# Kernel optimization log

Measured on AMD Instinct MI355X. Metric: run time of the kernel, lower is better.

The kernel has to match this reference:

```python
import jax, jax.numpy as jnp
import numpy as np
from jax import lax

K_NEI = 64      # max_num_neighbors in radius query
NEG = -1e30     # mask value for max-aggregation


def fps(pos, n_sample):
    """Farthest point sampling per cloud. pos: [B,N,3] -> idx [B,n_sample] int32.
    Deterministic start at point 0 (PyG uses a random start)."""
    B, N, _ = pos.shape
    start = jnp.zeros((B,), jnp.int32)
    big = jnp.full((B, N), jnp.finfo(pos.dtype).max, pos.dtype)
    def body(carry, _):
        mind, last = carry
        lp = jnp.take_along_axis(pos, last[:, None, None], axis=1)  # [B,1,3]
        d = jnp.sum((pos - lp) ** 2, -1)                            # [B,N]
        mind = jnp.minimum(mind, d)
        nxt = jnp.argmax(mind, axis=1).astype(jnp.int32)
        return (mind, nxt), nxt
    (_, _), rest = lax.scan(body, (big, start), None, length=n_sample - 1)
    return jnp.concatenate([start[None], rest], 0).T  # [B, n_sample]


def radius_nn(pos_all, pos_q, r, k):
    """Up to k nearest neighbors within radius r (per cloud).
    pos_all: [B,N,3], pos_q: [B,M,3] -> idx [B,M,k] int32, valid [B,M,k] bool."""
    d2 = jnp.sum((pos_q[:, :, None, :] - pos_all[:, None, :, :]) ** 2, -1)  # [B,M,N]
    score = jnp.where(d2 <= r * r, -d2, -jnp.inf)
    vals, idx = lax.top_k(score, k)
    return idx, jnp.isfinite(vals)


def gather(feat, idx):
    """feat: [B,P,C], idx: [B,M,k] -> [B,M,k,C]"""
    B, M, k = idx.shape
    out = jnp.take_along_axis(feat, idx.reshape(B, M * k)[:, :, None], axis=1)
    return out.reshape(B, M, k, feat.shape[-1])


def mlp3(x, w1, b1, w2, b2, w3, b3):
    x = jax.nn.relu(x @ w1 + b1)
    x = jax.nn.relu(x @ w2 + b2)
    return x @ w3 + b3


def point_conv(x, pos_src, pos_dst, nidx, valid, params):
    """PyG PointConv: message = local_nn([x_j, pos_j - pos_i]), max aggregation."""
    rel = gather(pos_src, nidx) - pos_dst[:, :, None, :]          # [B,M,k,3]
    msg = rel if x is None else jnp.concatenate([gather(x, nidx), rel], -1)
    h = mlp3(msg, *params)                                        # [B,M,k,C]
    h = jnp.where(valid[..., None], h, NEG)
    out = jnp.max(h, axis=2)
    return jnp.where(valid.any(2)[..., None], out, 0.0)


def setup_inputs() -> dict:
    key = jax.random.key(0)
    shapes = {
        'sa1_w1': (3, 64), 'sa1_b1': (64,), 'sa1_w2': (64, 64), 'sa1_b2': (64,),
        'sa1_w3': (64, 128), 'sa1_b3': (128,),
        'sa2_w1': (131, 128), 'sa2_b1': (128,), 'sa2_w2': (128, 128), 'sa2_b2': (128,),
        'sa2_w3': (128, 256), 'sa2_b3': (256,),
        'g_w1': (259, 256), 'g_b1': (256,), 'g_w2': (256, 512), 'g_b2': (512,),
        'g_w3': (512, 1024), 'g_b3': (1024,),
        'l1_w': (1024, 512), 'l1_b': (512,), 'l2_w': (512, 256), 'l2_b': (256,),
        'l3_w': (256, 7), 'l3_b': (7,),
    }
    ks = jax.random.split(key, len(shapes) + 1)
    inp = {'points': jax.random.uniform(ks[0], (8, 4096, 3), jnp.float32)}
    for i, (name, shp) in enumerate(shapes.items()):
        inp[name] = jax.random.normal(ks[i + 1], shp, jnp.float32) / np.sqrt(shp[0]).astype(np.float32)
    return inp


def reference(points, sa1_w1, sa1_b1, sa1_w2, sa1_b2, sa1_w3, sa1_b3,
              sa2_w1, sa2_b1, sa2_w2, sa2_b2, sa2_w3, sa2_b3,
              g_w1, g_b1, g_w2, g_b2, g_w3, g_b3,
              l1_w, l1_b, l2_w, l2_b, l3_w, l3_b):
    B, N, _ = points.shape
    pos = points[..., :3]
    # ---- stage 1: fps ratio 0.5, radius 0.1 ----
    N1 = N // 2
    idx1 = fps(pos, N1)
    pos1 = jnp.take_along_axis(pos, idx1[..., None], axis=1)      # [B,N1,3]
    nidx1, valid1 = radius_nn(pos, pos1, 0.1, K_NEI)
    x1 = jax.nn.relu(point_conv(None, pos, pos1, nidx1, valid1,
                                (sa1_w1, sa1_b1, sa1_w2, sa1_b2, sa1_w3, sa1_b3)))
    # ---- stage 2: fps ratio 0.25, radius 0.2 ----
    N2 = N1 // 4
    idx2 = fps(pos1, N2)
    pos2 = jnp.take_along_axis(pos1, idx2[..., None], axis=1)     # [B,N2,3]
    nidx2, valid2 = radius_nn(pos1, pos2, 0.2, K_NEI)
    x2 = jax.nn.relu(point_conv(x1, pos1, pos2, nidx2, valid2,
                                (sa2_w1, sa2_b1, sa2_w2, sa2_b2, sa2_w3, sa2_b3)))
    # ---- global MLP + grouped maxpool over 128 points ----
    g = mlp3(jnp.concatenate([x2, pos2], -1), g_w1, g_b1, g_w2, g_b2, g_w3, g_b3)  # [B,N2,1024]
    g = g.reshape(-1, 128, 1024).max(axis=1)                      # [B*N2/128, 1024]
    h = jax.nn.relu(g @ l1_w + l1_b)                              # dropout = identity (eval)
    h = jax.nn.relu(h @ l2_w + l2_b)
    h = h @ l3_w + l3_b                                           # [B*N2/128, 7]
    b_out = h.reshape(B, -1, 7).mean(axis=1)                      # [B,7]
    t = b_out[:, :3]
    q = b_out[:, 3:]
    q = q / jnp.maximum(jnp.linalg.norm(q, axis=-1, keepdims=True), 1e-12)
    return jnp.concatenate([t, q], axis=-1)
```

## Files before the change

kernel.cpp:

```cpp
#include <hip/hip_runtime.h>
#include <float.h>


typedef float f32x2 __attribute__((ext_vector_type(2)));

__device__ __forceinline__ float d2_rn(float ax, float ay, float az,
                                       float bx, float by, float bz) {
  float dx = __fsub_rn(ax, bx), dy = __fsub_rn(ay, by), dz = __fsub_rn(az, bz);
  return __fadd_rn(__fadd_rn(__fmul_rn(dx, dx), __fmul_rn(dy, dy)), __fmul_rn(dz, dz));
}

template<int CTRL>
__device__ __forceinline__ unsigned long long dppmax(unsigned long long a) {
  const unsigned int lo = (unsigned int)a, hi = (unsigned int)(a >> 32);
  const unsigned int slo =
      (unsigned int)__builtin_amdgcn_update_dpp(0, (int)lo, CTRL, 0xf, 0xf, true);
  const unsigned int shi =
      (unsigned int)__builtin_amdgcn_update_dpp(0, (int)hi, CTRL, 0xf, 0xf, true);
  const unsigned long long s = ((unsigned long long)shi << 32) | slo;
  return s > a ? s : a;
}

__device__ __forceinline__ unsigned int aload(const unsigned int* p) {
  return __hip_atomic_load(p, __ATOMIC_RELAXED, __HIP_MEMORY_SCOPE_AGENT);
}
__device__ __forceinline__ void astore(unsigned int* p, unsigned int v) {
  __hip_atomic_store(p, v, __ATOMIC_RELAXED, __HIP_MEMORY_SCOPE_AGENT);
}

__device__ __forceinline__ void barrier_lgkm() {
  asm volatile("s_waitcnt lgkmcnt(0)\n\ts_barrier" ::: "memory");
}

template<int N, int NS, int T>
__device__ void fps_core(float4* sxyz, int* s_idx,
                         unsigned long long* s_red,
                         float* __restrict__ outp,
                         unsigned int* __restrict__ pub) {
#pragma clang fp contract(off)
  constexpr int P = N / T;
  constexpr int P2 = P / 2;
  constexpr int W = T / 64;
  const int t = threadIdx.x;
  __builtin_amdgcn_s_setprio(2);
  f32x2 px[P2], py[P2], pz[P2], mind[P2];
  unsigned int kc0[P2], kc1[P2];
#pragma unroll
  for (int j = 0; j < P2; ++j) {
    const int i0 = (2*j)*T + t, i1 = i0 + T;
    const float4 c0 = sxyz[i0], c1 = sxyz[i1];
    px[j] = f32x2{c0.x, c1.x};
    py[j] = f32x2{c0.y, c1.y};
    pz[j] = f32x2{c0.z, c1.z};
    mind[j] = f32x2{FLT_MAX, FLT_MAX};
    kc0[j] = (unsigned int)(N - 1 - i0);
    kc1[j] = (unsigned int)(N - 1 - i1);
  }
  float lx = sxyz[0].x, ly = sxyz[0].y, lz = sxyz[0].z;
  if (t == 0) { s_idx[0] = 0; astore(&pub[0], 1u); }
  for (int it = 1; it < NS; ++it) {
    const f32x2 lx2 = {lx, lx}, ly2 = {ly, ly}, lz2 = {lz, lz};
    float bv0 = -1.0f, bv1 = -1.0f;
    unsigned int bk0 = 0, bk1 = 0;
#pragma unroll
    for (int j = 0; j < P2; ++j) {
      const f32x2 dx = px[j] - lx2;
      const f32x2 dy = py[j] - ly2;
      const f32x2 dz = pz[j] - lz2;
      const f32x2 s = ((dx*dx) + (dy*dy)) + (dz*dz);
      const float m0 = fminf(mind[j].x, s.x);
      const float m1 = fminf(mind[j].y, s.y);
      mind[j] = f32x2{m0, m1};
      const bool g0 = m0 > bv0;
      bv0 = g0 ? m0 : bv0; bk0 = g0 ? kc0[j] : bk0;
      const bool g1 = m1 > bv1;
      bv1 = g1 ? m1 : bv1; bk1 = g1 ? kc1[j] : bk1;
    }
    const unsigned long long k0 = ((unsigned long long)__float_as_uint(bv0) << 32) | bk0;
    const unsigned long long k1 = ((unsigned long long)__float_as_uint(bv1) << 32) | bk1;
    unsigned long long key = k0 > k1 ? k0 : k1;
    key = dppmax<0x111>(key);
    key = dppmax<0x112>(key);
    key = dppmax<0x114>(key);
    key = dppmax<0x118>(key);
    key = dppmax<0x142>(key);
    key = dppmax<0x143>(key);
    const int par = it & 1;
    if ((t & 63) == 63) s_red[par*W + (t >> 6)] = key;
    barrier_lgkm();
    unsigned long long best = s_red[par*W];
#pragma unroll
    for (int w = 1; w < W; ++w) {
      const unsigned long long o = s_red[par*W + w];
      best = o > best ? o : best;
    }
    const int idx = (N - 1) - (int)(unsigned int)(best & 0xFFFFFFFFull);
    if (t == 0) { astore(&pub[it], (unsigned int)(idx + 1)); s_idx[it] = idx; }
    const float4 c = sxyz[idx];
    lx = c.x; ly = c.y; lz = c.z;
  }
  __builtin_amdgcn_s_setprio(0);
  __syncthreads();
  for (int s = t; s < NS; s += T) {
    const float4 c = sxyz[s_idx[s]];
    outp[(size_t)s*3 + 0] = c.x; outp[(size_t)s*3 + 1] = c.y; outp[(size_t)s*3 + 2] = c.z;
  }
}

struct FpsSm { float4 xyz[4096]; int idx[2048]; unsigned long long red[8]; };
struct SmRC1 {
  union { struct { float d2[1024]; int id[1024]; } rad; float x[64 * 64]; } u;
  float rel[64 * 4];
  float out[128];
  int nid[64];
  int qidx;
  int cnt;
};
struct SmRC2 {
  union { struct { float d2[1024]; int id[1024]; } rad; float x[64 * 128]; } u;
  float rel[64 * 4];
  float out[256];
  int nid[64];
  int qidx;
  int cnt;
};
union Mega1Sm { FpsSm f; SmRC1 r; };

__device__ void rc1_item(int b, int m,
                         const float* __restrict__ points,
                         const unsigned int* __restrict__ sidx1, float r2,
                         const float* __restrict__ w1, const float* __restrict__ b1,
                         const float* __restrict__ w2, const float* __restrict__ b2,
                         const float* __restrict__ w3, const float* __restrict__ b3,
                         float* __restrict__ x1, SmRC1& R) {
  const int t = threadIdx.x;
  const int q = b*2048 + m;
  if (t == 0) {
    unsigned int v;
    while ((v = aload(&sidx1[q])) == 0u) __builtin_amdgcn_s_sleep(16);
    R.qidx = (int)v - 1;
    R.cnt = 0;
  }
  __syncthreads();
  const float* pb = points + (size_t)b * 4096 * 3;
  const int qi = R.qidx;
  const float qx = pb[qi*3], qy = pb[qi*3+1], qz = pb[qi*3+2];
  for (int i = t; i < 4096; i += 256) {
    const float d2 = d2_rn(qx, qy, qz, pb[i*3], pb[i*3+1], pb[i*3+2]);
    if (d2 <= r2) {
      const int p = atomicAdd(&R.cnt, 1);
      if (p < 1024) { R.u.rad.d2[p] = d2; R.u.rad.id[p] = i; }
    }
  }
  __syncthreads();
  const int cntc = min(R.cnt, 1024);
  const int cnt = min(cntc, 64);
  float* outp = x1 + (size_t)q * 128;
  if (cnt == 0) { if (t < 128) outp[t] = 0.f; return; }
  if (cntc <= 64) {
    if (t < cntc) R.nid[t] = R.u.rad.id[t];
  } else {
    for (int c = t; c < cntc; c += 256) {
      const float dc = R.u.rad.d2[c]; const int ic = R.u.rad.id[c];
      int rank = 0;
      for (int jj = 0; jj < cntc; ++jj)
        rank += (R.u.rad.d2[jj] < dc) || (R.u.rad.d2[jj] == dc && R.u.rad.id[jj] < ic);
      if (rank < 64) R.nid[rank] = ic;
    }
  }
  __syncthreads();
  if (t < 64) {
    const int n = (t < cnt) ? R.nid[t] : 0;
    const float* p = points + ((size_t)(b << 12) + n) * 3;
    R.rel[t*4+0] = p[0] - qx; R.rel[t*4+1] = p[1] - qy; R.rel[t*4+2] = p[2] - qz;
  }
  __syncthreads();
  const int j = t & 63;
  const int g = __builtin_amdgcn_readfirstlane(t >> 6);
  float* s_x = R.u.x;
  const int sw  = j & 31;
  const int row = j * 64;
  const float rx = R.rel[j*4+0], ry = R.rel[j*4+1], rz = R.rel[j*4+2];
  f32x2 acc[8];
  { const f32x2* bv = (const f32x2*)(b1 + g*16);
#pragma unroll
    for (int c = 0; c < 8; ++c) acc[c] = bv[c]; }
#pragma unroll
  for (int kk = 0; kk < 3; ++kk) {
    const float xk = (kk == 0) ? rx : ((kk == 1) ? ry : rz);
    const f32x2 xv = {xk, xk};
    const float4* wr = (const float4*)(w1 + kk*64 + g*16);
#pragma unroll
    for (int c4 = 0; c4 < 4; ++c4) {
      const float4 w = wr[c4];
      acc[c4*2+0] += xv * f32x2{w.x, w.y};
      acc[c4*2+1] += xv * f32x2{w.z, w.w};
    }
  }
#pragma unroll
  for (int c = 0; c < 8; ++c) {
    const f32x2 v = acc[c];
    s_x[row + ((g*16 + 2*c + 0) ^ sw)] = fmaxf(v.x, 0.f);
    s_x[row + ((g*16 + 2*c + 1) ^ sw)] = fmaxf(v.y, 0.f);
  }
  __syncthreads();
  { const f32x2* bv = (const f32x2*)(b2 + g*16);
#pragma unroll
    for (int c = 0; c < 8; ++c) acc[c] = bv[c]; }
#pragma unroll 2
  for (int k = 0; k < 64; ++k) {
    const float hk = s_x[row + (k ^ sw)];
    const f32x2 hv = {hk, hk};
    const float4* wr = (const float4*)(w2 + k*64 + g*16);
#pragma unroll
    for (int c4 = 0; c4 < 4; ++c4) {
      const float4 w = wr[c4];
      acc[c4*2+0] += hv * f32x2{w.x, w.y};
      acc[c4*2+1] += hv * f32x2{w.z, w.w};
    }
  }
  __syncthreads();
#pragma unroll
  for (int c = 0; c < 8; ++c) {
    const f32x2 v = acc[c];
    s_x[row + ((g*16 + 2*c + 0) ^ sw)] = fmaxf(v.x, 0.f);
    s_x[row + ((g*16 + 2*c + 1) ^ sw)] = fmaxf(v.y, 0.f);
  }
  __syncthreads();
#pragma unroll 1
  for (int p = 0; p < 2; ++p) {
    f32x2 a[8];
    { const f32x2* bv = (const f32x2*)(b3 + g*32 + p*16);
#pragma unroll
      for (int c = 0; c < 8; ++c) a[c] = bv[c]; }
#pragma unroll 2
    for (int k = 0; k < 64; ++k) {
      const float hk = s_x[row + (k ^ sw)];
      const f32x2 hv = {hk, hk};
      const float4* wr = (const float4*)(w3 + k*128 + g*32 + p*16);
#pragma unroll
      for (int c4 = 0; c4 < 4; ++c4) {
        const float4 w = wr[c4];
        a[c4*2+0] += hv * f32x2{w.x, w.y};
        a[c4*2+1] += hv * f32x2{w.z, w.w};
      }
    }
    if (j >= cnt) {
#pragma unroll
      for (int c = 0; c < 8; ++c) a[c] = f32x2{-1e30f, -1e30f};
    }
#pragma unroll
    for (int off = 32; off > 0; off >>= 1) {
#pragma unroll
      for (int c = 0; c < 8; ++c) {
        a[c].x = fmaxf(a[c].x, __shfl_xor(a[c].x, off, 64));
        a[c].y = fmaxf(a[c].y, __shfl_xor(a[c].y, off, 64));
      }
    }
    if (j == 0) {
#pragma unroll
      for (int c = 0; c < 8; ++c) *(f32x2*)(&R.out[g*32 + p*16 + 2*c]) = a[c];
    }
  }
  __syncthreads();
  if (t < 128) outp[t] = fmaxf(R.out[t], 0.f);
}

__global__ __launch_bounds__(256, 2) void mega1_kernel(
    const float* __restrict__ points, float* __restrict__ pos1,
    float* __restrict__ pos2,
    unsigned int* __restrict__ sidx1, unsigned int* __restrict__ sidx2,
    int* __restrict__ qhead, float r2,
    const float* __restrict__ w1, const float* __restrict__ b1,
    const float* __restrict__ w2, const float* __restrict__ b2,
    const float* __restrict__ w3, const float* __restrict__ b3,
    float* __restrict__ x1) {
  __shared__ Mega1Sm sm;
  __shared__ int s_item;
  const int t = threadIdx.x;
  for (;;) {
    __syncthreads();
    if (t == 0) s_item = atomicAdd(qhead, 1);
    __syncthreads();
    const int w = s_item;
    if (w >= 16 + 8*2048) return;
    if (w < 8) {
      const float* pb = points + (size_t)w * 4096 * 3;
      for (int i = t; i < 4096; i += 256)
        sm.f.xyz[i] = make_float4(pb[i*3], pb[i*3+1], pb[i*3+2], 0.f);
      __syncthreads();
      fps_core<4096, 2048, 256>(sm.f.xyz, sm.f.idx, sm.f.red,
                                pos1 + (size_t)w*2048*3, sidx1 + w*2048);
    } else if (w < 16) {
      const int b = w - 8;
      const float* pb = points + (size_t)b * 4096 * 3;
      for (int i = t; i < 2048; i += 256) {
        unsigned int v;
        while ((v = aload(&sidx1[b*2048 + i])) == 0u) __builtin_amdgcn_s_sleep(16);
        const int idx = (int)v - 1;
        sm.f.xyz[i] = make_float4(pb[idx*3], pb[idx*3+1], pb[idx*3+2], 0.f);
      }
      __syncthreads();
      fps_core<2048, 512, 256>(sm.f.xyz, sm.f.idx, sm.f.red,
                               pos2 + (size_t)b*512*3, sidx2 + b*512);
    } else {
      const int qq = w - 16;
      rc1_item(qq & 7, qq >> 3, points, sidx1, r2, w1, b1, w2, b2, w3, b3, x1, sm.r);
    }
  }
}

__global__ __launch_bounds__(256, 4) void rc2_kernel(
    const float* __restrict__ x1, const float* __restrict__ pos1,
    const unsigned int* __restrict__ sidx2, float r2,
    const float* __restrict__ w1, const float* __restrict__ b1,
    const float* __restrict__ w2, const float* __restrict__ b2,
    const float* __restrict__ w3, const float* __restrict__ b3,
    float* __restrict__ x2) {
  __shared__ SmRC2 R;
  const int q = blockIdx.x;
  const int b = q >> 9;
  const int t = threadIdx.x;
  if (t == 0) {
    unsigned int v;
    while ((v = aload(&sidx2[q])) == 0u) __builtin_amdgcn_s_sleep(16);
    R.qidx = (int)v - 1;
    R.cnt = 0;
  }
  __syncthreads();
  const float* pb = pos1 + (size_t)b * 2048 * 3;
  const int qi = R.qidx;
  const float qx = pb[qi*3], qy = pb[qi*3+1], qz = pb[qi*3+2];
  for (int i = t; i < 2048; i += 256) {
    const float d2 = d2_rn(qx, qy, qz, pb[i*3], pb[i*3+1], pb[i*3+2]);
    if (d2 <= r2) {
      const int p = atomicAdd(&R.cnt, 1);
      if (p < 1024) { R.u.rad.d2[p] = d2; R.u.rad.id[p] = i; }
    }
  }
  __syncthreads();
  const int cntc = min(R.cnt, 1024);
  const int cnt = min(cntc, 64);
  float* outp = x2 + (size_t)q * 256;
  if (cnt == 0) { outp[t] = 0.f; return; }
  if (cntc <= 64) {
    if (t < cntc) R.nid[t] = R.u.rad.id[t];
  } else {
    for (int c = t; c < cntc; c += 256) {
      const float dc = R.u.rad.d2[c]; const int ic = R.u.rad.id[c];
      int rank = 0;
      for (int jj = 0; jj < cntc; ++jj)
        rank += (R.u.rad.d2[jj] < dc) || (R.u.rad.d2[jj] == dc && R.u.rad.id[jj] < ic);
      if (rank < 64) R.nid[rank] = ic;
    }
  }
  __syncthreads();
  if (t < 64) {
    const int n = (t < cnt) ? R.nid[t] : 0;
    const float* p = pos1 + ((size_t)(b << 11) + n) * 3;
    R.rel[t*4+0] = p[0] - qx; R.rel[t*4+1] = p[1] - qy; R.rel[t*4+2] = p[2] - qz;
  }
  __syncthreads();
  float* s_x = R.u.x;
  for (int i = t; i < 64*128; i += 256) {
    const int r = i >> 7, c = i & 127;
    const int n = ((r < cnt) ? R.nid[r] : 0);
    s_x[r*128 + (c ^ (r & 31))] = x1[((size_t)(b << 11) + n)*128 + c];
  }
  __syncthreads();
  const int j = t & 63;
  const int g = __builtin_amdgcn_readfirstlane(t >> 6);
  const int sw  = j & 31;
  const int row = j * 128;
  f32x2 acc[16];
  { const f32x2* bv = (const f32x2*)(b1 + g*32);
#pragma unroll
    for (int c = 0; c < 16; ++c) acc[c] = bv[c]; }
#pragma unroll 2
  for (int k = 0; k < 128; ++k) {
    const float xk = s_x[row + (k ^ sw)];
    const f32x2 xv = {xk, xk};
    const float4* wr = (const float4*)(w1 + k*128 + g*32);
#pragma unroll
    for (int c4 = 0; c4 < 8; ++c4) {
      const float4 w = wr[c4];
      acc[c4*2+0] += xv * f32x2{w.x, w.y};
      acc[c4*2+1] += xv * f32x2{w.z, w.w};
    }
  }
#pragma unroll
  for (int kk = 0; kk < 3; ++kk) {
    const float xk = R.rel[j*4 + kk];
    const f32x2 xv = {xk, xk};
    const float4* wr = (const float4*)(w1 + (128 + kk)*128 + g*32);
#pragma unroll
    for (int c4 = 0; c4 < 8; ++c4) {
      const float4 w = wr[c4];
      acc[c4*2+0] += xv * f32x2{w.x, w.y};
      acc[c4*2+1] += xv * f32x2{w.z, w.w};
    }
  }
  __syncthreads();
#pragma unroll
  for (int c = 0; c < 16; ++c) {
    const f32x2 v = acc[c];
    s_x[row + ((g*32 + 2*c + 0) ^ sw)] = fmaxf(v.x, 0.f);
    s_x[row + ((g*32 + 2*c + 1) ^ sw)] = fmaxf(v.y, 0.f);
  }
  __syncthreads();
  { const f32x2* bv = (const f32x2*)(b2 + g*32);
#pragma unroll
    for (int c = 0; c < 16; ++c) acc[c] = bv[c]; }
#pragma unroll 2
  for (int k = 0; k < 128; ++k) {
    const float hk = s_x[row + (k ^ sw)];
    const f32x2 hv = {hk, hk};
    const float4* wr = (const float4*)(w2 + k*128 + g*32);
#pragma unroll
    for (int c4 = 0; c4 < 8; ++c4) {
      const float4 w = wr[c4];
      acc[c4*2+0] += hv * f32x2{w.x, w.y};
      acc[c4*2+1] += hv * f32x2{w.z, w.w};
    }
  }
  __syncthreads();
#pragma unroll
  for (int c = 0; c < 16; ++c) {
    const f32x2 v = acc[c];
    s_x[row + ((g*32 + 2*c + 0) ^ sw)] = fmaxf(v.x, 0.f);
    s_x[row + ((g*32 + 2*c + 1) ^ sw)] = fmaxf(v.y, 0.f);
  }
  __syncthreads();
#pragma unroll 1
  for (int p = 0; p < 2; ++p) {
    f32x2 a[16];
    { const f32x2* bv = (const f32x2*)(b3 + g*64 + p*32);
#pragma unroll
      for (int c = 0; c < 16; ++c) a[c] = bv[c]; }
#pragma unroll 2
    for (int k = 0; k < 128; ++k) {
      const float hk = s_x[row + (k ^ sw)];
      const f32x2 hv = {hk, hk};
      const float4* wr = (const float4*)(w3 + k*256 + g*64 + p*32);
#pragma unroll
      for (int c4 = 0; c4 < 8; ++c4) {
        const float4 w = wr[c4];
        a[c4*2+0] += hv * f32x2{w.x, w.y};
        a[c4*2+1] += hv * f32x2{w.z, w.w};
      }
    }
    if (j >= cnt) {
#pragma unroll
      for (int c = 0; c < 16; ++c) a[c] = f32x2{-1e30f, -1e30f};
    }
#pragma unroll
    for (int off = 32; off > 0; off >>= 1) {
#pragma unroll
      for (int c = 0; c < 16; ++c) {
        a[c].x = fmaxf(a[c].x, __shfl_xor(a[c].x, off, 64));
        a[c].y = fmaxf(a[c].y, __shfl_xor(a[c].y, off, 64));
      }
    }
    if (j == 0) {
#pragma unroll
      for (int c = 0; c < 16; ++c) *(f32x2*)(&R.out[g*64 + p*32 + 2*c]) = a[c];
    }
  }
  __syncthreads();
  outp[t] = fmaxf(R.out[t], 0.f);
}

__global__ __launch_bounds__(256) void gmlp_kernel(
    const float* __restrict__ x2, const float* __restrict__ pos2,
    const float* __restrict__ w1, const float* __restrict__ b1,
    const float* __restrict__ w2, const float* __restrict__ b2,
    const float* __restrict__ w3, const float* __restrict__ b3,
    float* __restrict__ gpart) {
  const int blk = blockIdx.x;
  const int t = threadIdx.x;
  __shared__ float sA[260 * 18];
  __shared__ float sB[512 * 18];
  const int p0 = blk * 16;
  for (int i = t; i < 16*256; i += 256) {
    const int p = i >> 8, k = i & 255;
    sA[k*18 + p] = x2[(size_t)(p0 + p)*256 + k];
  }
  if (t < 48) { const int p = t/3, c = t%3; sA[(256+c)*18 + p] = pos2[(size_t)(p0+p)*3 + c]; }
  __syncthreads();
  f32x2 h1[8];
  { const float bb = b1[t];
#pragma unroll
    for (int p8 = 0; p8 < 8; ++p8) h1[p8] = f32x2{bb, bb}; }
#pragma unroll 2
  for (int k = 0; k < 259; ++k) {
    const float w = w1[(size_t)k*256 + t];
    const f32x2 wv = {w, w};
    const f32x2* row = (const f32x2*)(&sA[k*18]);
#pragma unroll
    for (int p8 = 0; p8 < 8; ++p8) h1[p8] += row[p8] * wv;
  }
  __syncthreads();
#pragma unroll
  for (int p8 = 0; p8 < 8; ++p8) {
    f32x2 a = h1[p8];
    a.x = fmaxf(a.x, 0.f); a.y = fmaxf(a.y, 0.f);
    *(f32x2*)(&sA[t*18 + 2*p8]) = a;
  }
  __syncthreads();
  f32x2 h2a[8], h2b[8];
  { const float ba = b2[t], bb = b2[t + 256];
#pragma unroll
    for (int p8 = 0; p8 < 8; ++p8) { h2a[p8] = f32x2{ba, ba}; h2b[p8] = f32x2{bb, bb}; } }
#pragma unroll 2
  for (int k = 0; k < 256; ++k) {
    const float wa = w2[(size_t)k*512 + t];
    const float wb = w2[(size_t)k*512 + t + 256];
    const f32x2 wav = {wa, wa}, wbv = {wb, wb};
    const f32x2* row = (const f32x2*)(&sA[k*18]);
#pragma unroll
    for (int p8 = 0; p8 < 8; ++p8) { const f32x2 x = row[p8]; h2a[p8] += x*wav; h2b[p8] += x*wbv; }
  }
  __syncthreads();
#pragma unroll
  for (int p8 = 0; p8 < 8; ++p8) {
    f32x2 a = h2a[p8], c = h2b[p8];
    a.x = fmaxf(a.x, 0.f); a.y = fmaxf(a.y, 0.f);
    c.x = fmaxf(c.x, 0.f); c.y = fmaxf(c.y, 0.f);
    *(f32x2*)(&sB[t*18 + 2*p8]) = a;
    *(f32x2*)(&sB[(t+256)*18 + 2*p8]) = c;
  }
  __syncthreads();
  f32x2 a3[4][8];
#pragma unroll
  for (int c = 0; c < 4; ++c) {
    const float bb = b3[t + c*256];
#pragma unroll
    for (int p8 = 0; p8 < 8; ++p8) a3[c][p8] = f32x2{bb, bb};
  }
#pragma unroll 2
  for (int k = 0; k < 512; ++k) {
    const f32x2* row = (const f32x2*)(&sB[k*18]);
    f32x2 xk[8];
#pragma unroll
    for (int p8 = 0; p8 < 8; ++p8) xk[p8] = row[p8];
#pragma unroll
    for (int c = 0; c < 4; ++c) {
      const float w = w3[(size_t)k*1024 + t + c*256];
      const f32x2 wv = {w, w};
#pragma unroll
      for (int p8 = 0; p8 < 8; ++p8) a3[c][p8] += xk[p8] * wv;
    }
  }
#pragma unroll
  for (int c = 0; c < 4; ++c) {
    f32x2 m2 = a3[c][0];
#pragma unroll
    for (int p8 = 1; p8 < 8; ++p8) {
      m2.x = fmaxf(m2.x, a3[c][p8].x); m2.y = fmaxf(m2.y, a3[c][p8].y);
    }
    gpart[(size_t)blk*1024 + t + c*256] = fmaxf(m2.x, m2.y);
  }
}

__global__ __launch_bounds__(256) void head_kernel(
    const float* __restrict__ gpart,
    const float* __restrict__ l1w, const float* __restrict__ l1b,
    const float* __restrict__ l2w, const float* __restrict__ l2b,
    const float* __restrict__ l3w, const float* __restrict__ l3b,
    float* __restrict__ h3) {
  const int r = blockIdx.x, t = threadIdx.x;
  __shared__ float sIn[1024];
  __shared__ float sH[512];
  __shared__ float sH2[256];
  for (int i = t; i < 1024; i += 256) {
    float v = gpart[(size_t)(r*8)*1024 + i];
#pragma unroll
    for (int rr = 1; rr < 8; ++rr) v = fmaxf(v, gpart[(size_t)(r*8 + rr)*1024 + i]);
    sIn[i] = v;
  }
  __syncthreads();
  float a0 = l1b[t], a1 = l1b[t + 256];
#pragma unroll 4
  for (int k = 0; k < 1024; ++k) {
    const float x = sIn[k];
    a0 += x * l1w[(size_t)k*512 + t];
    a1 += x * l1w[(size_t)k*512 + t + 256];
  }
  sH[t] = fmaxf(a0, 0.f); sH[t+256] = fmaxf(a1, 0.f);
  __syncthreads();
  float a = l2b[t];
#pragma unroll 4
  for (int k = 0; k < 512; ++k) a += sH[k] * l2w[(size_t)k*256 + t];
  sH2[t] = fmaxf(a, 0.f);
  __syncthreads();
  if (t < 7) {
    float acc = l3b[t];
#pragma unroll 4
    for (int k = 0; k < 256; ++k) acc += sH2[k] * l3w[(size_t)k*7 + t];
    h3[(size_t)r*7 + t] = acc;
  }
}

__global__ void final_kernel(const float* __restrict__ h3, float* __restrict__ out) {
  const int b = threadIdx.x;
  if (b >= 8) return;
  float v[7];
#pragma unroll
  for (int c = 0; c < 7; ++c) {
    const float s = ((h3[(b*4+0)*7+c] + h3[(b*4+1)*7+c]) + h3[(b*4+2)*7+c]) + h3[(b*4+3)*7+c];
    v[c] = s * 0.25f;
  }
  const float nrm = fmaxf(sqrtf(((v[3]*v[3] + v[4]*v[4]) + v[5]*v[5]) + v[6]*v[6]), 1e-12f);
  out[b*7+0] = v[0]; out[b*7+1] = v[1]; out[b*7+2] = v[2];
  out[b*7+3] = v[3]/nrm; out[b*7+4] = v[4]/nrm;
  out[b*7+5] = v[5]/nrm; out[b*7+6] = v[6]/nrm;
}

extern "C" void kernel_launch(void* const* d_in, const int* in_sizes, int n_in,
                              void* d_out, int out_size, void* d_ws, size_t ws_size,
                              hipStream_t stream) {
  const float* points = (const float*)d_in[0];
  const float* sa1_w1 = (const float*)d_in[1];
  const float* sa1_b1 = (const float*)d_in[2];
  const float* sa1_w2 = (const float*)d_in[3];
  const float* sa1_b2 = (const float*)d_in[4];
  const float* sa1_w3 = (const float*)d_in[5];
  const float* sa1_b3 = (const float*)d_in[6];
  const float* sa2_w1 = (const float*)d_in[7];
  const float* sa2_b1 = (const float*)d_in[8];
  const float* sa2_w2 = (const float*)d_in[9];
  const float* sa2_b2 = (const float*)d_in[10];
  const float* sa2_w3 = (const float*)d_in[11];
  const float* sa2_b3 = (const float*)d_in[12];
  const float* g_w1   = (const float*)d_in[13];
  const float* g_b1   = (const float*)d_in[14];
  const float* g_w2   = (const float*)d_in[15];
  const float* g_b2   = (const float*)d_in[16];
  const float* g_w3   = (const float*)d_in[17];
  const float* g_b3   = (const float*)d_in[18];
  const float* l1_w   = (const float*)d_in[19];
  const float* l1_b   = (const float*)d_in[20];
  const float* l2_w   = (const float*)d_in[21];
  const float* l2_b   = (const float*)d_in[22];
  const float* l3_w   = (const float*)d_in[23];
  const float* l3_b   = (const float*)d_in[24];

  unsigned int* u = (unsigned int*)d_ws;
  unsigned int* sidx1 = u;
  unsigned int* sidx2 = u + 16384;
  int* qhead1 = (int*)(u + 16384 + 4096);
  const size_t syncWords = 16384 + 4096 + 1;

  float* ws = (float*)d_ws + 20608;
  size_t o = 0;
  float* pos1  = ws + o; o += (size_t)8*2048*3;
  float* pos2  = ws + o; o += (size_t)8*512*3;
  float* x1    = ws + o; o += (size_t)8*2048*128;
  float* x2    = ws + o; o += (size_t)8*512*256;
  float* gpart = ws + o; o += (size_t)256*1024;
  float* h3    = ws + o; o += (size_t)32*7;

  hipMemsetAsync(d_ws, 0, syncWords * 4, stream);

  const float R2_1 = (float)(0.1 * 0.1);
  const float R2_2 = (float)(0.2 * 0.2);

  mega1_kernel<<<512, 256, 0, stream>>>(points, pos1, pos2, sidx1, sidx2, qhead1, R2_1,
                                        sa1_w1, sa1_b1, sa1_w2, sa1_b2, sa1_w3, sa1_b3, x1);
  rc2_kernel<<<8*512, 256, 0, stream>>>(x1, pos1, sidx2, R2_2,
                                        sa2_w1, sa2_b1, sa2_w2, sa2_b2, sa2_w3, sa2_b3, x2);
  gmlp_kernel<<<256, 256, 0, stream>>>(x2, pos2, g_w1, g_b1, g_w2, g_b2, g_w3, g_b3, gpart);
  head_kernel<<<32, 256, 0, stream>>>(gpart, l1_w, l1_b, l2_w, l2_b, l3_w, l3_b, h3);
  final_kernel<<<1, 64, 0, stream>>>(h3, (float*)d_out);
}
```

Measured before the change: 2.281 ms.

## Run FPS on a single wavefront to drop block barriers

The farthest-point-sampling loop now runs on one 64-lane wavefront instead of four waves per block. The per-iteration LDS cross-wave reduction and s_barrier are replaced by a readlane of the DPP-reduced key. Candidate indices are computed on the fly rather than held in registers. Each lane now handles four times as many points, which adds serial ALU work per iteration, and launch bounds drop to one block per SIMD to allow the larger register footprint, which may reduce occupancy for the rc1 items sharing the kernel.

```diff
diff --git a/kernel.cpp b/kernel.cpp
--- a/kernel.cpp
+++ b/kernel.cpp
@@ -28,34 +28,25 @@
   __hip_atomic_store(p, v, __ATOMIC_RELAXED, __HIP_MEMORY_SCOPE_AGENT);
 }
 
-__device__ __forceinline__ void barrier_lgkm() {
-  asm volatile("s_waitcnt lgkmcnt(0)\n\ts_barrier" ::: "memory");
-}
-
-template<int N, int NS, int T>
-__device__ void fps_core(float4* sxyz, int* s_idx,
-                         unsigned long long* s_red,
-                         float* __restrict__ outp,
-                         unsigned int* __restrict__ pub) {
+template<int N, int NS>
+__device__ void fps_core_sw(const float4* sxyz, int* s_idx,
+                            float* __restrict__ outp,
+                            unsigned int* __restrict__ pub) {
 #pragma clang fp contract(off)
-  constexpr int P = N / T;
-  constexpr int P2 = P / 2;
-  constexpr int W = T / 64;
+  constexpr int P2 = N / 128;
   const int t = threadIdx.x;
   __builtin_amdgcn_s_setprio(2);
   f32x2 px[P2], py[P2], pz[P2], mind[P2];
-  unsigned int kc0[P2], kc1[P2];
 #pragma unroll
   for (int j = 0; j < P2; ++j) {
-    const int i0 = (2*j)*T + t, i1 = i0 + T;
+    const int i0 = (2*j)*64 + t, i1 = i0 + 64;
     const float4 c0 = sxyz[i0], c1 = sxyz[i1];
     px[j] = f32x2{c0.x, c1.x};
     py[j] = f32x2{c0.y, c1.y};
     pz[j] = f32x2{c0.z, c1.z};
     mind[j] = f32x2{FLT_MAX, FLT_MAX};
-    kc0[j] = (unsigned int)(N - 1 - i0);
-    kc1[j] = (unsigned int)(N - 1 - i1);
-  }
+  }
+  const unsigned int baseKc = (unsigned int)(N - 1 - t);
   float lx = sxyz[0].x, ly = sxyz[0].y, lz = sxyz[0].z;
   if (t == 0) { s_idx[0] = 0; astore(&pub[0], 1u); }
   for (int it = 1; it < NS; ++it) {
@@ -71,10 +62,11 @@
       const float m0 = fminf(mind[j].x, s.x);
       const float m1 = fminf(mind[j].y, s.y);
       mind[j] = f32x2{m0, m1};
+      const unsigned int kci0 = baseKc - (unsigned int)(128*j);
       const bool g0 = m0 > bv0;
-      bv0 = g0 ? m0 : bv0; bk0 = g0 ? kc0[j] : bk0;
+      bv0 = g0 ? m0 : bv0; bk0 = g0 ? kci0 : bk0;
       const bool g1 = m1 > bv1;
-      bv1 = g1 ? m1 : bv1; bk1 = g1 ? kc1[j] : bk1;
+      bv1 = g1 ? m1 : bv1; bk1 = g1 ? (kci0 - 64u) : bk1;
     }
     const unsigned long long k0 = ((unsigned long long)__float_as_uint(bv0) << 32) | bk0;
     const unsigned long long k1 = ((unsigned long long)__float_as_uint(bv1) << 32) | bk1;
@@ -85,29 +77,21 @@
     key = dppmax<0x118>(key);
     key = dppmax<0x142>(key);
     key = dppmax<0x143>(key);
-    const int par = it & 1;
-    if ((t & 63) == 63) s_red[par*W + (t >> 6)] = key;
-    barrier_lgkm();
-    unsigned long long best = s_red[par*W];
-#pragma unroll
-    for (int w = 1; w < W; ++w) {
-      const unsigned long long o = s_red[par*W + w];
-      best = o > best ? o : best;
-    }
-    const int idx = (N - 1) - (int)(unsigned int)(best & 0xFFFFFFFFull);
+    const unsigned int kc =
+        (unsigned int)__builtin_amdgcn_readlane((int)(unsigned int)key, 63);
+    const int idx = (N - 1) - (int)kc;
     if (t == 0) { astore(&pub[it], (unsigned int)(idx + 1)); s_idx[it] = idx; }
     const float4 c = sxyz[idx];
     lx = c.x; ly = c.y; lz = c.z;
   }
   __builtin_amdgcn_s_setprio(0);
-  __syncthreads();
-  for (int s = t; s < NS; s += T) {
+  for (int s = t; s < NS; s += 64) {
     const float4 c = sxyz[s_idx[s]];
     outp[(size_t)s*3 + 0] = c.x; outp[(size_t)s*3 + 1] = c.y; outp[(size_t)s*3 + 2] = c.z;
   }
 }
 
-struct FpsSm { float4 xyz[4096]; int idx[2048]; unsigned long long red[8]; };
+struct FpsSm { float4 xyz[4096]; int idx[2048]; };
 struct SmRC1 {
   union { struct { float d2[1024]; int id[1024]; } rad; float x[64 * 64]; } u;
   float rel[64 * 4];
@@ -266,7 +250,7 @@
   if (t < 128) outp[t] = fmaxf(R.out[t], 0.f);
 }
 
-__global__ __launch_bounds__(256, 2) void mega1_kernel(
+__global__ __launch_bounds__(256, 1) void mega1_kernel(
     const float* __restrict__ points, float* __restrict__ pos1,
     float* __restrict__ pos2,
     unsigned int* __restrict__ sidx1, unsigned int* __restrict__ sidx2,
@@ -289,7 +273,8 @@
       for (int i = t; i < 4096; i += 256)
         sm.f.xyz[i] = make_float4(pb[i*3], pb[i*3+1], pb[i*3+2], 0.f);
       __syncthreads();
-      fps_core<4096, 2048, 256>(sm.f.xyz, sm.f.idx, sm.f.red,
+      if (t < 64)
+        fps_core_sw<4096, 2048>(sm.f.xyz, sm.f.idx,
                                 pos1 + (size_t)w*2048*3, sidx1 + w*2048);
     } else if (w < 16) {
       const int b = w - 8;
@@ -301,7 +286,8 @@
         sm.f.xyz[i] = make_float4(pb[idx*3], pb[idx*3+1], pb[idx*3+2], 0.f);
       }
       __syncthreads();
-      fps_core<2048, 512, 256>(sm.f.xyz, sm.f.idx, sm.f.red,
+      if (t < 64)
+        fps_core_sw<2048, 512>(sm.f.xyz, sm.f.idx,
                                pos2 + (size_t)b*512*3, sidx2 + b*512);
     } else {
       const int qq = w - 16;
```

Result: slower. 4.333 ms (+89.9%).
